# Performance work log

Measured on AMD Instinct MI355X. Metric: run time of the kernel, lower is better.

The kernel has to match this reference:

```python
import jax, jax.numpy as jnp
import numpy as np

N, U, V = 512, 2048, 43          # batch, phoneme seq len, vocab (Phoneme43)
H, K, NCLASS = 512, 10, 512      # hidden, GMM components, 2**bit
EPS = 1e-5


def gru_cell(x, h, wih, whh, bih, bhh):
    # PyTorch GRU gate order: r, z, n
    gi = x @ wih.T + bih          # [N, 3H]
    gh = h @ whh.T + bhh          # [N, 3H]
    gi_r, gi_z, gi_n = jnp.split(gi, 3, axis=1)
    gh_r, gh_z, gh_n = jnp.split(gh, 3, axis=1)
    r = jax.nn.sigmoid(gi_r + gh_r)
    z = jax.nn.sigmoid(gi_z + gh_z)
    n = jnp.tanh(gi_n + r * gh_n)
    return (1.0 - z) * n + z * h


def setup_inputs() -> dict:
    key = jax.random.key(0)
    ks = jax.random.split(key, 20)
    s = 0.05  # keep exp() arguments tame
    inp = {
        "xt": jax.random.normal(ks[0], (N,), jnp.float32),
        "cx": jax.random.uniform(ks[1], (N, U, V), jnp.float32),
        "encoder_hidden": jax.random.normal(ks[2], (1, N, H), jnp.float32),
        "wt_1": jax.random.normal(ks[3], (N, V), jnp.float32) * s,
        "h2t_1": jax.random.normal(ks[4], (1, N, H), jnp.float32),
        "h3t_1": jax.random.uniform(ks[5], (1, N, H), jnp.float32),
        "kappa_t_1": jax.random.uniform(ks[6], (N, K), jnp.float32),
        # learned params
        "Wh1p_w": jax.random.normal(ks[7], (3 * K, H + V), jnp.float32) * s,
        "Wh1p_b": jax.random.normal(ks[8], (3 * K,), jnp.float32) * s,
        "rnn2_wih": jax.random.normal(ks[9], (3 * H, 1 + V), jnp.float32) * s,
        "rnn2_whh": jax.random.normal(ks[10], (3 * H, H), jnp.float32) * s,
        "rnn2_bih": jax.random.normal(ks[11], (3 * H,), jnp.float32) * s,
        "rnn2_bhh": jax.random.normal(ks[12], (3 * H,), jnp.float32) * s,
        "rnn3_wih": jax.random.normal(ks[13], (3 * H, H), jnp.float32) * s,
        "rnn3_whh": jax.random.normal(ks[14], (3 * H, H), jnp.float32) * s,
        "rnn3_bih": jax.random.normal(ks[15], (3 * H,), jnp.float32) * s,
        "rnn3_bhh": jax.random.normal(ks[16], (3 * H,), jnp.float32) * s,
        "Y_w": jax.random.normal(ks[17], (NCLASS, H), jnp.float32) * s,
        "Y_b": jax.random.normal(ks[18], (NCLASS,), jnp.float32) * s,
    }
    return inp


def reference(xt, cx, encoder_hidden, wt_1, h2t_1, h3t_1, kappa_t_1,
              Wh1p_w, Wh1p_b, rnn2_wih, rnn2_whh, rnn2_bih, rnn2_bhh,
              rnn3_wih, rnn3_whh, rnn3_bih, rnn3_bhh, Y_w, Y_b):
    eh = encoder_hidden[0]                                   # [N, H]
    abk = jnp.concatenate([eh, wt_1], axis=1) @ Wh1p_w.T + Wh1p_b  # [N, 3K]
    alpha = jnp.exp(abk[:, :K]) + EPS                        # [N, K]
    beta = jnp.exp(abk[:, K:2 * K]) + EPS                    # [N, K]
    kappa = kappa_t_1 + jnp.exp(abk[:, 2 * K:3 * K])         # [N, K]
    u = jnp.arange(cx.shape[1], dtype=cx.dtype)              # [U]
    # Graves GMM attention window: phi[n,u] = sum_k alpha * exp(-beta*(kappa-u)^2)
    phi = jnp.sum(alpha[:, :, None] *
                  jnp.exp(-beta[:, :, None] * (kappa[:, :, None] - u) ** 2),
                  axis=1)                                    # [N, U]
    wt = jnp.einsum("nuv,nu->nv", cx, phi)                  # [N, V]
    x2 = jnp.concatenate([xt[:, None], wt], axis=1)          # [N, 1+V]
    h2 = gru_cell(x2, h2t_1[0], rnn2_wih, rnn2_whh, rnn2_bih, rnn2_bhh)
    res = h2
    h3 = gru_cell(jax.nn.relu(h2), h3t_1[0], rnn3_wih, rnn3_whh, rnn3_bih, rnn3_bhh)
    out = h3 + res                                           # [N, H]
    dist = jax.nn.relu(out) @ Y_w.T + Y_b                    # [N, n_class]
    dist = dist[:, None, :]                                  # [N, 1, n_class] (transpose(0,1) of [1,N,C])
    return dist, h2[None], h3[None], phi, wt, kappa
```

## Files before the change

### kernel.cpp

```cpp
#include <hip/hip_runtime.h>
#include <math.h>

typedef unsigned short ushortT;
typedef __attribute__((ext_vector_type(8))) short bf16x8;
typedef __attribute__((ext_vector_type(8))) unsigned short u16x8;
typedef __attribute__((ext_vector_type(4))) float f32x4;
typedef float f32x4u __attribute__((ext_vector_type(4), aligned(4)));

#define NN   512
#define UU   2048
#define VV   43
#define HH   512
#define KMIX 10
#define NCLS 512
#define EPSF 1e-5f
#define KCAT 555
#define PLANE 262144

#define OFF_DIST  0
#define OFF_H2    262144
#define OFF_H3    524288
#define OFF_PHI   786432
#define OFF_WT    1835008
#define OFF_KAPPA 1857024

__device__ __forceinline__ ushortT f2bf(float f) {
    unsigned int u = __builtin_bit_cast(unsigned int, f);
    u = (u + 0x7fffu + ((u >> 16) & 1u)) >> 16;
    return (ushortT)u;
}

__device__ __forceinline__ u16x8 cv8(float4 lo, float4 hi) {
    u16x8 o;
    o[0]=f2bf(lo.x); o[1]=f2bf(lo.y); o[2]=f2bf(lo.z); o[3]=f2bf(lo.w);
    o[4]=f2bf(hi.x); o[5]=f2bf(hi.y); o[6]=f2bf(hi.z); o[7]=f2bf(hi.w);
    return o;
}

struct AttnS {
    float x[KCAT];
    float sm[32];
    float aL[KMIX], bL[KMIX], kL[KMIX], um[KMIX];
    float red[4*VV];
    float wtv[VV+1];
};

template<int NG, int NSA, int NSB, int EPI, int WIK, int MODE>
__device__ __forceinline__ void gemm_body(
    int bj0, int bm0, ushortT* lds0, ushortT* lds1,
    const ushortT* __restrict__ Ai, const float* __restrict__ Wi,
    const float* __restrict__ Ah, const float* __restrict__ Wh,
    const float* __restrict__ bih, const float* __restrict__ bhh,
    const float* __restrict__ hprev, const float* __restrict__ resv,
    float* __restrict__ outF, ushortT* __restrict__ outB,
    const float* __restrict__ Yb, float* __restrict__ preC)
{
    constexpr int NS = NSA + NSB;
    int tid = threadIdx.x, lane = tid & 63, wid = tid >> 6;
    int wm = wid >> 1, wj = wid & 1;
    int fcol = lane & 15, g2 = lane >> 4;
    int arow = tid >> 3, aslot = tid & 7;

    float4 stgA[NG+1][2], stgB[NG+1][2];
    const float4 fz = {0.f, 0.f, 0.f, 0.f};

    auto loadregs = [&](int s, float4 (&dst)[NG+1][2]) {
        if (s < NSA) {
            dst[0][0] = *(const float4*)(Ai + (size_t)(bm0 + arow)*(NSA*64) + s*64 + aslot*8);
#pragma unroll
            for (int q = 1; q <= NG; ++q) {
                int unit = (q-1)*256 + tid;
                int brow = unit >> 3, bslot = unit & 7;
                int gate = brow >> 5, r = brow & 31;
                int col = s*64 + bslot*8;
                const float* src = Wi + (size_t)(gate*512 + bj0 + r)*WIK + col;
                if constexpr (WIK % 64 != 0) {
                    dst[q][0] = (col + 4 <= WIK) ? *(const float4*)src : fz;
                    dst[q][1] = (col + 8 <= WIK) ? *(const float4*)(src + 4) : fz;
                } else {
                    dst[q][0] = *(const float4*)src;
                    dst[q][1] = *(const float4*)(src + 4);
                }
            }
        } else {
            int kb = (s - NSA)*64;
            const float* srcA = Ah + (size_t)(bm0 + arow)*512 + kb + aslot*8;
            dst[0][0] = *(const float4*)srcA;
            dst[0][1] = *(const float4*)(srcA + 4);
#pragma unroll
            for (int q = 1; q <= NG; ++q) {
                int unit = (q-1)*256 + tid;
                int brow = unit >> 3, bslot = unit & 7;
                int gate = brow >> 5, r = brow & 31;
                const float* src = Wh + (size_t)(gate*512 + bj0 + r)*512 + kb + bslot*8;
                dst[q][0] = *(const float4*)src;
                dst[q][1] = *(const float4*)(src + 4);
            }
        }
    };
    auto stow = [&](int s, const float4 (&src)[NG+1][2], ushortT* buf) {
        if (s < NSA) {
            *(float4*)(buf + arow*64 + (aslot ^ (arow & 7))*8) = src[0][0];
        } else {
            *(u16x8*)(buf + arow*64 + (aslot ^ (arow & 7))*8) = cv8(src[0][0], src[0][1]);
        }
#pragma unroll
        for (int q = 1; q <= NG; ++q) {
            int unit = (q-1)*256 + tid;
            int brow = unit >> 3, bslot = unit & 7;
            *(u16x8*)(buf + 2048 + brow*64 + (bslot ^ (brow & 7))*8) = cv8(src[q][0], src[q][1]);
        }
    };

    f32x4 aR = {0.f,0.f,0.f,0.f}, aZ = {0.f,0.f,0.f,0.f};
    f32x4 aN1 = {0.f,0.f,0.f,0.f}, aN2 = {0.f,0.f,0.f,0.f};

    int ra = wm*16 + fcol, rb = wj*16 + fcol;

    loadregs(0, stgA);
    stow(0, stgA, lds0);
    if (NS > 1) loadregs(1, stgB);
    __syncthreads();

#pragma unroll
    for (int s = 0; s < NS; ++s) {
        ushortT* cur = (s & 1) ? lds1 : lds0;
        ushortT* nxt = (s & 1) ? lds0 : lds1;
        if (s + 2 < NS) {
            if (s & 1) loadregs(s + 2, stgB); else loadregs(s + 2, stgA);
        }
        bf16x8 af0 = *(const bf16x8*)(cur + ra*64 + ((g2    ) ^ (ra & 7))*8);
        bf16x8 af1 = *(const bf16x8*)(cur + ra*64 + ((4 + g2) ^ (ra & 7))*8);
        bf16x8 b0[NG], b1[NG];
#pragma unroll
        for (int g = 0; g < NG; ++g) {
            int rbt = g*32 + rb;
            b0[g] = *(const bf16x8*)(cur + 2048 + rbt*64 + ((g2    ) ^ (rbt & 7))*8);
            b1[g] = *(const bf16x8*)(cur + 2048 + rbt*64 + ((4 + g2) ^ (rbt & 7))*8);
        }
        if (s + 1 < NS) {
            if (s & 1) stow(s + 1, stgA, nxt); else stow(s + 1, stgB, nxt);
        }
        aR = __builtin_amdgcn_mfma_f32_16x16x32_bf16(af0, b0[0], aR, 0, 0, 0);
        aR = __builtin_amdgcn_mfma_f32_16x16x32_bf16(af1, b1[0], aR, 0, 0, 0);
        if constexpr (NG >= 2) {
            aZ = __builtin_amdgcn_mfma_f32_16x16x32_bf16(af0, b0[1], aZ, 0, 0, 0);
            aZ = __builtin_amdgcn_mfma_f32_16x16x32_bf16(af1, b1[1], aZ, 0, 0, 0);
        }
        if constexpr (NG >= 3) {
            if (s < NSA) {
                aN1 = __builtin_amdgcn_mfma_f32_16x16x32_bf16(af0, b0[2], aN1, 0, 0, 0);
                aN1 = __builtin_amdgcn_mfma_f32_16x16x32_bf16(af1, b1[2], aN1, 0, 0, 0);
            } else {
                aN2 = __builtin_amdgcn_mfma_f32_16x16x32_bf16(af0, b0[2], aN2, 0, 0, 0);
                aN2 = __builtin_amdgcn_mfma_f32_16x16x32_bf16(af1, b1[2], aN2, 0, 0, 0);
            }
        }
        __syncthreads();
    }

    int row0 = bm0 + wm*16 + (lane >> 4)*4;
    int col  = bj0 + wj*16 + fcol;

    if constexpr (MODE == 1) {
#pragma unroll
        for (int e = 0; e < 4; ++e) {
            size_t off = (size_t)(row0 + e)*512 + col;
            preC[off]           = aR[e];
            preC[PLANE + off]   = aZ[e];
            preC[2*PLANE + off] = aN2[e];
        }
    } else if constexpr (EPI == 0) {
        float b = Yb[col];
#pragma unroll
        for (int e = 0; e < 4; ++e)
            outF[(size_t)(row0 + e)*512 + col] = aR[e] + b;
    } else {
        float b_r  = bih[col] + bhh[col];
        float b_z  = bih[512 + col] + bhh[512 + col];
        float b_ni = bih[1024 + col];
        float b_nh = bhh[1024 + col];
#pragma unroll
        for (int e = 0; e < 4; ++e) {
            size_t off = (size_t)(row0 + e)*512 + col;
            float gr = aR[e], gz = aZ[e], gnh = aN2[e];
            if constexpr (MODE == 2) {
                gr  += preC[off];
                gz  += preC[PLANE + off];
                gnh  = preC[2*PLANE + off];
            }
            float r  = 1.f/(1.f + __expf(-(gr + b_r)));
            float z  = 1.f/(1.f + __expf(-(gz + b_z)));
            float nn = tanhf(aN1[e] + b_ni + r*(gnh + b_nh));
            float h  = (1.f - z)*nn + z*hprev[off];
            outF[off] = h;
            float xo = (EPI == 2) ? (h + resv[off]) : h;
            outB[off] = f2bf(fmaxf(xo, 0.f));
        }
    }
}

__global__ __launch_bounds__(256) void attn_gh(
    const float* __restrict__ xt, const float* __restrict__ cx,
    const float* __restrict__ eh, const float* __restrict__ wt_1,
    const float* __restrict__ Ww, const float* __restrict__ Wb,
    const float* __restrict__ kappa_prev,
    float* __restrict__ phi_out, float* __restrict__ wt_out,
    float* __restrict__ kappa_out, ushortT* __restrict__ A2,
    const float* __restrict__ h2p, const float* __restrict__ w2hh,
    const float* __restrict__ h3p, const float* __restrict__ w3hh,
    float* __restrict__ gh2C, float* __restrict__ gh3C)
{
    __shared__ __align__(16) ushortT smem[2][4*32*64];
    int bb = blockIdx.x, t = threadIdx.x;

    if (bb >= NN) {
        int gb = bb - NN;
        int sub = gb & 255;
        int bj0 = (sub & 15)*32, bm0 = (sub >> 4)*32;
        if (gb < 256)
            gemm_body<3, 0, 8, 1, 512, 1>(bj0, bm0, &smem[0][0], &smem[1][0],
                nullptr, nullptr, h2p, w2hh, nullptr, nullptr, nullptr, nullptr,
                nullptr, nullptr, nullptr, gh2C);
        else
            gemm_body<3, 0, 8, 1, 512, 1>(bj0, bm0, &smem[0][0], &smem[1][0],
                nullptr, nullptr, h3p, w3hh, nullptr, nullptr, nullptr, nullptr,
                nullptr, nullptr, nullptr, gh3C);
        return;
    }

    AttnS* S = (AttnS*)&smem[0][0];
    int n = bb;
    int lane = t & 63, wid = t >> 6;
    const float* cxn = cx + (size_t)n*UU*VV;

    const float* rowp0 = cxn + (size_t)t*VV;
    f32x4u r0[10]; f32x4u rt0;
#pragma unroll
    for (int q = 0; q < 10; ++q) r0[q] = *(const f32x4u*)(rowp0 + q*4);
    rt0 = *(const f32x4u*)(rowp0 + 39);

    for (int i = t; i < KCAT; i += 256)
        S->x[i] = (i < HH) ? eh[(size_t)n*HH + i] : wt_1[n*VV + (i - HH)];
    __syncthreads();
#pragma unroll
    for (int rr = 0; rr < 8; ++rr) {
        int g = rr*4 + wid;
        float v = 0.f;
        if (g < 30) {
            const float* w = Ww + (size_t)g*KCAT;
#pragma unroll
            for (int q = 0; q < 9; ++q) {
                int i = q*64 + lane;
                if (i < KCAT) v += S->x[i]*w[i];
            }
        }
        v += __shfl_xor(v, 32, 64); v += __shfl_xor(v, 16, 64); v += __shfl_xor(v, 8, 64);
        v += __shfl_xor(v, 4, 64);  v += __shfl_xor(v, 2, 64);  v += __shfl_xor(v, 1, 64);
        if (lane == 0 && g < 30) S->sm[g] = v;
    }
    __syncthreads();
    if (t < 30) {
        float ev = __expf(S->sm[t] + Wb[t]);
        if (t < 10)       S->aL[t] = ev + EPSF;
        else if (t < 20)  S->bL[t-10] = ev + EPSF;
        else { float kap = kappa_prev[n*KMIX + (t-20)] + ev; S->kL[t-20] = kap;
               kappa_out[n*KMIX + (t-20)] = kap; }
    }
    __syncthreads();
    if (t < KMIX)
        S->um[t] = S->kL[t] + sqrtf(fmaxf(60.f + __logf(S->aL[t]), 0.f) / S->bL[t]);
    __syncthreads();
    float ulim = S->um[0];
#pragma unroll
    for (int k = 1; k < KMIX; ++k) ulim = fmaxf(ulim, S->um[k]);
    int nchunks = min(8, (int)(ulim) / 256 + 1);
    nchunks = __builtin_amdgcn_readfirstlane(nchunks);

    float aL[KMIX], bL[KMIX], kL[KMIX];
#pragma unroll
    for (int k = 0; k < KMIX; ++k) { aL[k] = S->aL[k]; bL[k] = S->bL[k]; kL[k] = S->kL[k]; }

    float phi_reg[8];
#pragma unroll
    for (int c = 0; c < 8; ++c) {
        int u = c*256 + t; float uu = (float)u, s = 0.f;
#pragma unroll
        for (int k = 0; k < KMIX; ++k) { float d = kL[k] - uu; s += aL[k]*__expf(-bL[k]*d*d); }
        phi_reg[c] = s;
        phi_out[(size_t)n*UU + u] = s;
    }

    float acc[VV];
    {
        float p = phi_reg[0];
#pragma unroll
        for (int q = 0; q < 10; ++q) {
            acc[q*4+0] = r0[q].x*p; acc[q*4+1] = r0[q].y*p;
            acc[q*4+2] = r0[q].z*p; acc[q*4+3] = r0[q].w*p;
        }
        acc[40] = rt0.y*p; acc[41] = rt0.z*p; acc[42] = rt0.w*p;
    }
#pragma unroll
    for (int c = 1; c < 8; ++c) {
        if (c < nchunks) {
            const float* rowp = cxn + (size_t)(c*256 + t)*VV;
            f32x4u r[10];
#pragma unroll
            for (int q = 0; q < 10; ++q) r[q] = *(const f32x4u*)(rowp + q*4);
            f32x4u rt = *(const f32x4u*)(rowp + 39);
            float p = phi_reg[c];
#pragma unroll
            for (int q = 0; q < 10; ++q) {
                acc[q*4+0] += r[q].x*p; acc[q*4+1] += r[q].y*p;
                acc[q*4+2] += r[q].z*p; acc[q*4+3] += r[q].w*p;
            }
            acc[40] += rt.y*p; acc[41] += rt.z*p; acc[42] += rt.w*p;
        }
    }

#pragma unroll
    for (int v = 0; v < VV; ++v) {
        float val = acc[v];
#pragma unroll
        for (int off = 32; off > 0; off >>= 1) val += __shfl_down(val, off, 64);
        if (lane == 0) S->red[wid*VV + v] = val;
    }
    __syncthreads();
    if (t < VV) {
        float w4 = S->red[t] + S->red[VV+t] + S->red[2*VV+t] + S->red[3*VV+t];
        wt_out[n*VV + t] = w4; S->wtv[t] = w4;
    }
    __syncthreads();
    if (t < 64) {
        float v = (t == 0) ? xt[n] : (t < 44 ? S->wtv[t-1] : 0.f);
        A2[(size_t)n*64 + t] = f2bf(v);
    }
}

template<int NG, int NSA, int NSB, int EPI, int WIK, int MODE>
__global__ __launch_bounds__(256) void gemm_k(
    const ushortT* __restrict__ Ai, const float* __restrict__ Wi,
    const float* __restrict__ Ah, const float* __restrict__ Wh,
    const float* __restrict__ bih, const float* __restrict__ bhh,
    const float* __restrict__ hprev, const float* __restrict__ resv,
    float* __restrict__ outF, ushortT* __restrict__ outB,
    const float* __restrict__ Yb, float* __restrict__ preC)
{
    __shared__ __align__(16) ushortT lds0[(NG+1)*32*64];
    __shared__ __align__(16) ushortT lds1[(NG+1)*32*64];
    gemm_body<NG, NSA, NSB, EPI, WIK, MODE>(
        blockIdx.x*32, blockIdx.y*32, lds0, lds1,
        Ai, Wi, Ah, Wh, bih, bhh, hprev, resv, outF, outB, Yb, preC);
}

extern "C" void kernel_launch(void* const* d_in, const int* in_sizes, int n_in,
                              void* d_out, int out_size, void* d_ws, size_t ws_size,
                              hipStream_t stream)
{
    const float* xt   = (const float*)d_in[0];
    const float* cx   = (const float*)d_in[1];
    const float* eh   = (const float*)d_in[2];
    const float* wt_1 = (const float*)d_in[3];
    const float* h2p  = (const float*)d_in[4];
    const float* h3p  = (const float*)d_in[5];
    const float* kp   = (const float*)d_in[6];
    const float* Ww   = (const float*)d_in[7];
    const float* Wb   = (const float*)d_in[8];
    const float* w2ih = (const float*)d_in[9];
    const float* w2hh = (const float*)d_in[10];
    const float* b2ih = (const float*)d_in[11];
    const float* b2hh = (const float*)d_in[12];
    const float* w3ih = (const float*)d_in[13];
    const float* w3hh = (const float*)d_in[14];
    const float* b3ih = (const float*)d_in[15];
    const float* b3hh = (const float*)d_in[16];
    const float* Yw   = (const float*)d_in[17];
    const float* Yb   = (const float*)d_in[18];

    float* out = (float*)d_out;
    float* dist = out + OFF_DIST;
    float* h2o  = out + OFF_H2;
    float* h3o  = out + OFF_H3;
    float* phi  = out + OFF_PHI;
    float* wto  = out + OFF_WT;
    float* kapo = out + OFF_KAPPA;

    char* p = (char*)d_ws;
    ushortT* A2   = (ushortT*)p;  p += (size_t)512*64*2;
    ushortT* A3i  = (ushortT*)p;  p += (size_t)512*512*2;
    ushortT* Ad   = (ushortT*)p;  p += (size_t)512*512*2;
    float*   gh2C = (float*)p;    p += (size_t)3*PLANE*4;
    float*   gh3C = (float*)p;    p += (size_t)3*PLANE*4;

    attn_gh<<<1024, 256, 0, stream>>>(
        xt, cx, eh, wt_1, Ww, Wb, kp, phi, wto, kapo, A2,
        h2p, w2hh, h3p, w3hh, gh2C, gh3C);
    gemm_k<3, 1, 0, 1, 44, 2><<<dim3(16, 16), 256, 0, stream>>>(
        A2, w2ih, nullptr, nullptr, b2ih, b2hh, h2p, nullptr, h2o, A3i, nullptr, gh2C);
    gemm_k<3, 8, 0, 2, 512, 2><<<dim3(16, 16), 256, 0, stream>>>(
        A3i, w3ih, nullptr, nullptr, b3ih, b3hh, h3p, h2o, h3o, Ad, nullptr, gh3C);
    gemm_k<1, 8, 0, 0, 512, 0><<<dim3(16, 16), 256, 0, stream>>>(
        Ad, Yw, nullptr, nullptr, nullptr, nullptr, nullptr, nullptr, dist, nullptr, Yb, nullptr);
}
```

Before: 50.75 us.

## Fuse GRU2 and GRU3 into one kernel and skip negligible phi chunks

```diff
diff --git a/kernel.cpp b/kernel.cpp
--- a/kernel.cpp
+++ b/kernel.cpp
@@ -44,6 +44,8 @@
     float red[4*VV];
     float wtv[VV+1];
 };
+
+#define MFMA16(a,b,c) __builtin_amdgcn_mfma_f32_16x16x32_bf16(a,b,c,0,0,0)
 
 template<int NG, int NSA, int NSB, int EPI, int WIK, int MODE>
 __device__ __forceinline__ void gemm_body(
@@ -141,19 +143,19 @@
         if (s + 1 < NS) {
             if (s & 1) stow(s + 1, stgA, nxt); else stow(s + 1, stgB, nxt);
         }
-        aR = __builtin_amdgcn_mfma_f32_16x16x32_bf16(af0, b0[0], aR, 0, 0, 0);
-        aR = __builtin_amdgcn_mfma_f32_16x16x32_bf16(af1, b1[0], aR, 0, 0, 0);
+        aR = MFMA16(af0, b0[0], aR);
+        aR = MFMA16(af1, b1[0], aR);
         if constexpr (NG >= 2) {
-            aZ = __builtin_amdgcn_mfma_f32_16x16x32_bf16(af0, b0[1], aZ, 0, 0, 0);
-            aZ = __builtin_amdgcn_mfma_f32_16x16x32_bf16(af1, b1[1], aZ, 0, 0, 0);
+            aZ = MFMA16(af0, b0[1], aZ);
+            aZ = MFMA16(af1, b1[1], aZ);
         }
         if constexpr (NG >= 3) {
             if (s < NSA) {
-                aN1 = __builtin_amdgcn_mfma_f32_16x16x32_bf16(af0, b0[2], aN1, 0, 0, 0);
-                aN1 = __builtin_amdgcn_mfma_f32_16x16x32_bf16(af1, b1[2], aN1, 0, 0, 0);
+                aN1 = MFMA16(af0, b0[2], aN1);
+                aN1 = MFMA16(af1, b1[2], aN1);
             } else {
-                aN2 = __builtin_amdgcn_mfma_f32_16x16x32_bf16(af0, b0[2], aN2, 0, 0, 0);
-                aN2 = __builtin_amdgcn_mfma_f32_16x16x32_bf16(af1, b1[2], aN2, 0, 0, 0);
+                aN2 = MFMA16(af0, b0[2], aN2);
+                aN2 = MFMA16(af1, b1[2], aN2);
             }
         }
         __syncthreads();
@@ -284,11 +286,14 @@
     float phi_reg[8];
 #pragma unroll
     for (int c = 0; c < 8; ++c) {
-        int u = c*256 + t; float uu = (float)u, s = 0.f;
-#pragma unroll
-        for (int k = 0; k < KMIX; ++k) { float d = kL[k] - uu; s += aL[k]*__expf(-bL[k]*d*d); }
+        float s = 0.f;
+        if ((float)(c*256 + wid*64) <= ulim) {
+            int u = c*256 + t; float uu = (float)u;
+#pragma unroll
+            for (int k = 0; k < KMIX; ++k) { float d = kL[k] - uu; s += aL[k]*__expf(-bL[k]*d*d); }
+        }
         phi_reg[c] = s;
-        phi_out[(size_t)n*UU + u] = s;
+        phi_out[(size_t)n*UU + c*256 + t] = s;
     }
 
     float acc[VV];
@@ -335,6 +340,173 @@
     if (t < 64) {
         float v = (t == 0) ? xt[n] : (t < 44 ? S->wtv[t-1] : 0.f);
         A2[(size_t)n*64 + t] = f2bf(v);
+    }
+}
+
+__global__ __launch_bounds__(256) void gru23_kernel(
+    const ushortT* __restrict__ A2, const float* __restrict__ w2ih,
+    const float* __restrict__ gh2C, const float* __restrict__ b2ih,
+    const float* __restrict__ b2hh, const float* __restrict__ h2p,
+    const float* __restrict__ w3ih, const float* __restrict__ gh3C,
+    const float* __restrict__ b3ih, const float* __restrict__ b3hh,
+    const float* __restrict__ h3p, float* __restrict__ h2o,
+    float* __restrict__ h3o, ushortT* __restrict__ Ad)
+{
+    __shared__ __align__(16) ushortT A3[8*2048];
+    __shared__ __align__(16) ushortT lB0[96*64];
+    __shared__ __align__(16) ushortT lB1[96*64];
+    __shared__ __align__(16) ushortT lA2[32*64];
+
+    int tid = threadIdx.x, lane = tid & 63, wid = tid >> 6;
+    int wm = wid >> 1, wj = wid & 1;
+    int bx = blockIdx.x;
+    int bj0 = bx*32, bm0 = blockIdx.y*32;
+    int fcol = lane & 15, g2 = lane >> 4;
+    int arow = tid >> 3, aslot = tid & 7;
+    const float4 fz = {0.f,0.f,0.f,0.f};
+
+    float4 regA[3][2], regB[3][2];
+
+    auto loadB2 = [&](int jj, float4 (&d)[3][2]) {
+#pragma unroll
+        for (int q = 0; q < 3; ++q) {
+            int unit = q*256 + tid;
+            int brow = unit >> 3, bslot = unit & 7;
+            int gate = brow >> 5, r = brow & 31;
+            int col = bslot*8;
+            const float* src = w2ih + (size_t)(gate*512 + jj*32 + r)*44 + col;
+            d[q][0] = *(const float4*)src;
+            d[q][1] = (col + 8 <= 44) ? *(const float4*)(src + 4) : fz;
+        }
+    };
+    auto loadB3 = [&](int s, float4 (&d)[3][2]) {
+#pragma unroll
+        for (int q = 0; q < 3; ++q) {
+            int unit = q*256 + tid;
+            int brow = unit >> 3, bslot = unit & 7;
+            int gate = brow >> 5, r = brow & 31;
+            const float* src = w3ih + (size_t)(gate*512 + bj0 + r)*512 + s*64 + bslot*8;
+            d[q][0] = *(const float4*)src;
+            d[q][1] = *(const float4*)(src + 4);
+        }
+    };
+    auto stowB = [&](const float4 (&s)[3][2], ushortT* buf) {
+#pragma unroll
+        for (int q = 0; q < 3; ++q) {
+            int unit = q*256 + tid;
+            int brow = unit >> 3, bslot = unit & 7;
+            *(u16x8*)(buf + brow*64 + (bslot ^ (brow & 7))*8) = cv8(s[q][0], s[q][1]);
+        }
+    };
+
+    {
+        float4 v = *(const float4*)(A2 + (size_t)(bm0 + arow)*64 + aslot*8);
+        *(float4*)(lA2 + arow*64 + (aslot ^ (arow & 7))*8) = v;
+    }
+
+    int ra = wm*16 + fcol, rb = wj*16 + fcol;
+    int row0 = bm0 + wm*16 + (lane >> 4)*4;
+    int lr0  = wm*16 + (lane >> 4)*4;
+    float res4[4];
+
+    loadB2(0, regA);
+    stowB(regA, lB0);
+    loadB2(1, regB);
+    __syncthreads();
+
+    bf16x8 af0 = *(const bf16x8*)(lA2 + ra*64 + ((g2    ) ^ (ra & 7))*8);
+    bf16x8 af1 = *(const bf16x8*)(lA2 + ra*64 + ((4 + g2) ^ (ra & 7))*8);
+
+#pragma unroll 2
+    for (int jj = 0; jj < 16; ++jj) {
+        ushortT* cur = (jj & 1) ? lB1 : lB0;
+        ushortT* nxt = (jj & 1) ? lB0 : lB1;
+        int col = jj*32 + wj*16 + fcol;
+        float b_r  = b2ih[col] + b2hh[col];
+        float b_z  = b2ih[512 + col] + b2hh[512 + col];
+        float b_ni = b2ih[1024 + col];
+        float b_nh = b2hh[1024 + col];
+        float g2r[4], g2z[4], g2n[4], hp[4];
+#pragma unroll
+        for (int e = 0; e < 4; ++e) {
+            size_t off = (size_t)(row0 + e)*512 + col;
+            g2r[e] = gh2C[off]; g2z[e] = gh2C[PLANE + off]; g2n[e] = gh2C[2*PLANE + off];
+            hp[e]  = h2p[off];
+        }
+        if (jj + 2 < 16) { if (jj & 1) loadB2(jj + 2, regB); else loadB2(jj + 2, regA); }
+        bf16x8 b0[3], b1[3];
+#pragma unroll
+        for (int g = 0; g < 3; ++g) {
+            int rbt = g*32 + rb;
+            b0[g] = *(const bf16x8*)(cur + rbt*64 + ((g2    ) ^ (rbt & 7))*8);
+            b1[g] = *(const bf16x8*)(cur + rbt*64 + ((4 + g2) ^ (rbt & 7))*8);
+        }
+        if (jj + 1 < 16) { if (jj & 1) stowB(regA, nxt); else stowB(regB, nxt); }
+        f32x4 pR = {0.f,0.f,0.f,0.f}, pZ = {0.f,0.f,0.f,0.f}, pN = {0.f,0.f,0.f,0.f};
+        pR = MFMA16(af0, b0[0], pR); pR = MFMA16(af1, b1[0], pR);
+        pZ = MFMA16(af0, b0[1], pZ); pZ = MFMA16(af1, b1[1], pZ);
+        pN = MFMA16(af0, b0[2], pN); pN = MFMA16(af1, b1[2], pN);
+#pragma unroll
+        for (int e = 0; e < 4; ++e) {
+            float r  = 1.f/(1.f + __expf(-(pR[e] + g2r[e] + b_r)));
+            float z  = 1.f/(1.f + __expf(-(pZ[e] + g2z[e] + b_z)));
+            float nn = tanhf(pN[e] + b_ni + r*(g2n[e] + b_nh));
+            float h  = (1.f - z)*nn + z*hp[e];
+            if (bx == 0) h2o[(size_t)(row0 + e)*512 + col] = h;
+            if (jj == bx) res4[e] = h;
+            ushortT hb = f2bf(fmaxf(h, 0.f));
+            int ks = col >> 6, c6 = col & 63, slot = c6 >> 3, e8 = c6 & 7;
+            int lr = lr0 + e;
+            A3[ks*2048 + lr*64 + ((slot ^ (lr & 7))*8 + e8)] = hb;
+        }
+        __syncthreads();
+    }
+
+    f32x4 aR = {0.f,0.f,0.f,0.f}, aZ = {0.f,0.f,0.f,0.f}, aN1 = {0.f,0.f,0.f,0.f};
+    loadB3(0, regA);
+    stowB(regA, lB0);
+    loadB3(1, regB);
+    __syncthreads();
+#pragma unroll 2
+    for (int s = 0; s < 8; ++s) {
+        ushortT* cur = (s & 1) ? lB1 : lB0;
+        ushortT* nxt = (s & 1) ? lB0 : lB1;
+        if (s + 2 < 8) { if (s & 1) loadB3(s + 2, regB); else loadB3(s + 2, regA); }
+        bf16x8 a0 = *(const bf16x8*)(A3 + s*2048 + ra*64 + ((g2    ) ^ (ra & 7))*8);
+        bf16x8 a1 = *(const bf16x8*)(A3 + s*2048 + ra*64 + ((4 + g2) ^ (ra & 7))*8);
+        bf16x8 b0[3], b1[3];
+#pragma unroll
+        for (int g = 0; g < 3; ++g) {
+            int rbt = g*32 + rb;
+            b0[g] = *(const bf16x8*)(cur + rbt*64 + ((g2    ) ^ (rbt & 7))*8);
+            b1[g] = *(const bf16x8*)(cur + rbt*64 + ((4 + g2) ^ (rbt & 7))*8);
+        }
+        if (s + 1 < 8) { if (s & 1) stowB(regA, nxt); else stowB(regB, nxt); }
+        aR  = MFMA16(a0, b0[0], aR);  aR  = MFMA16(a1, b1[0], aR);
+        aZ  = MFMA16(a0, b0[1], aZ);  aZ  = MFMA16(a1, b1[1], aZ);
+        aN1 = MFMA16(a0, b0[2], aN1); aN1 = MFMA16(a1, b1[2], aN1);
+        __syncthreads();
+    }
+
+    {
+        int col = bj0 + wj*16 + fcol;
+        float b_r  = b3ih[col] + b3hh[col];
+        float b_z  = b3ih[512 + col] + b3hh[512 + col];
+        float b_ni = b3ih[1024 + col];
+        float b_nh = b3hh[1024 + col];
+#pragma unroll
+        for (int e = 0; e < 4; ++e) {
+            size_t off = (size_t)(row0 + e)*512 + col;
+            float gr  = aR[e]  + gh3C[off];
+            float gz  = aZ[e]  + gh3C[PLANE + off];
+            float gnh = gh3C[2*PLANE + off];
+            float r  = 1.f/(1.f + __expf(-(gr + b_r)));
+            float z  = 1.f/(1.f + __expf(-(gz + b_z)));
+            float nn = tanhf(aN1[e] + b_ni + r*(gnh + b_nh));
+            float h  = (1.f - z)*nn + z*h3p[off];
+            h3o[off] = h;
+            Ad[off]  = f2bf(fmaxf(h + res4[e], 0.f));
+        }
     }
 }
 
@@ -388,7 +560,6 @@
 
     char* p = (char*)d_ws;
     ushortT* A2   = (ushortT*)p;  p += (size_t)512*64*2;
-    ushortT* A3i  = (ushortT*)p;  p += (size_t)512*512*2;
     ushortT* Ad   = (ushortT*)p;  p += (size_t)512*512*2;
     float*   gh2C = (float*)p;    p += (size_t)3*PLANE*4;
     float*   gh3C = (float*)p;    p += (size_t)3*PLANE*4;
@@ -396,10 +567,9 @@
     attn_gh<<<1024, 256, 0, stream>>>(
         xt, cx, eh, wt_1, Ww, Wb, kp, phi, wto, kapo, A2,
         h2p, w2hh, h3p, w3hh, gh2C, gh3C);
-    gemm_k<3, 1, 0, 1, 44, 2><<<dim3(16, 16), 256, 0, stream>>>(
-        A2, w2ih, nullptr, nullptr, b2ih, b2hh, h2p, nullptr, h2o, A3i, nullptr, gh2C);
-    gemm_k<3, 8, 0, 2, 512, 2><<<dim3(16, 16), 256, 0, stream>>>(
-        A3i, w3ih, nullptr, nullptr, b3ih, b3hh, h3p, h2o, h3o, Ad, nullptr, gh3C);
+    gru23_kernel<<<dim3(16, 16), 256, 0, stream>>>(
+        A2, w2ih, gh2C, b2ih, b2hh, h2p,
+        w3ih, gh3C, b3ih, b3hh, h3p, h2o, h3o, Ad);
     gemm_k<1, 8, 0, 0, 512, 0><<<dim3(16, 16), 256, 0, stream>>>(
         Ad, Yw, nullptr, nullptr, nullptr, nullptr, nullptr, nullptr, dist, nullptr, Yb, nullptr);
 }
```

Measured after the change: 70.08 us. +38.1%, slower.
